# Performance work log

Measured on AMD Instinct MI355X. Metric: run time of the kernel, lower is better.

## Reference

```python
import jax, jax.numpy as jnp
import numpy as np

P_DROP = 0.2
N_NODES = 100000
N_EDGES = 1600000
IN_DIM, HID_DIM, OUT_DIM = 128, 128, 64


def sage_conv(x, src, dst, Wl, Wr, b, n_nodes):
    # PyG SAGEConv (aggr='mean', root_weight=True):
    #   out_i = W_l @ mean_{j in N(i)} x_j + W_r @ x_i + b
    msgs = jnp.take(x, src, axis=0)                                   # [E, d]
    agg = jax.ops.segment_sum(msgs, dst, num_segments=n_nodes)        # [N, d]
    cnt = jax.ops.segment_sum(jnp.ones((src.shape[0],), x.dtype), dst,
                              num_segments=n_nodes)                   # [N]
    agg = agg / jnp.maximum(cnt, 1.0)[:, None]                        # mean, 0 for isolated nodes
    return agg @ Wl + x @ Wr + b


def setup_inputs() -> dict:
    key = jax.random.key(0)
    ks = jax.random.split(key, 8)
    x = jax.random.normal(ks[0], (N_NODES, IN_DIM), dtype=jnp.float32)
    edge_index = jax.random.randint(ks[1], (2, N_EDGES), 0, N_NODES, dtype=jnp.int32)
    drop_u = jax.random.uniform(ks[2], (N_NODES, HID_DIM), dtype=jnp.float32)
    s1 = 1.0 / np.sqrt(IN_DIM)
    s2 = 1.0 / np.sqrt(HID_DIM)
    W1l = jax.random.normal(ks[3], (IN_DIM, HID_DIM), dtype=jnp.float32) * s1
    W1r = jax.random.normal(ks[4], (IN_DIM, HID_DIM), dtype=jnp.float32) * s1
    b1 = jnp.zeros((HID_DIM,), dtype=jnp.float32)
    W2l = jax.random.normal(ks[5], (HID_DIM, OUT_DIM), dtype=jnp.float32) * s2
    W2r = jax.random.normal(ks[6], (HID_DIM, OUT_DIM), dtype=jnp.float32) * s2
    b2 = jnp.zeros((OUT_DIM,), dtype=jnp.float32)
    return {"x": x, "edge_index": edge_index, "drop_u": drop_u,
            "W1l": W1l, "W1r": W1r, "b1": b1,
            "W2l": W2l, "W2r": W2r, "b2": b2}


def reference(x, edge_index, drop_u, W1l, W1r, b1, W2l, W2r, b2):
    n = x.shape[0]
    src, dst = edge_index[0], edge_index[1]
    h = jax.nn.elu(sage_conv(x, src, dst, W1l, W1r, b1, n))
    keep = (drop_u >= P_DROP).astype(h.dtype) / (1.0 - P_DROP)  # inverted dropout, p=0.2
    h = h * keep
    h = jax.nn.elu(sage_conv(h, src, dst, W2l, W2r, b2, n))
    return h
```

## Files before the change

kernel.cpp:

```cpp
#include <hip/hip_runtime.h>
#include <cstdint>
#include <cstddef>

#define TPB 256
#define BCAP 2560
#define NBKMAX 800
#define EPB 8192

typedef short bf16x8 __attribute__((ext_vector_type(8)));
typedef float f32x4 __attribute__((ext_vector_type(4)));

__device__ __forceinline__ unsigned short f2bf(float f) {
  unsigned int u = __float_as_uint(f);
  unsigned int r = (u + 0x7fffu + ((u >> 16) & 1u)) >> 16;
  return (unsigned short)r;
}
__device__ __forceinline__ float bf2f(unsigned short h) {
  return __uint_as_float(((unsigned int)h) << 16);
}

__device__ __forceinline__ float elu_neg(float v) { return __expf(v) - 1.0f; }

__device__ __forceinline__ void gload16(const void* g, void* l) {
  __builtin_amdgcn_global_load_lds(
      (const __attribute__((address_space(1))) unsigned int*)g,
      (__attribute__((address_space(3))) unsigned int*)l, 16, 0, 0);
}

template <int N>
__device__ __forceinline__ void waitvm() {
  asm volatile("s_waitcnt vmcnt(%0)" ::"n"(N) : "memory");
}


__global__ __launch_bounds__(256) void multisplit_scatter(
    const int* __restrict__ src, const int* __restrict__ dst,
    unsigned int* __restrict__ be, int* __restrict__ bcnt, int e, int nbk) {
  __shared__ int hist[NBKMAX];
  __shared__ int curs[NBKMAX];
  int tx = threadIdx.x;
  int e0 = blockIdx.x * EPB;
  int e1 = min(e, e0 + EPB);

  for (int b = tx; b < nbk; b += TPB) hist[b] = 0;
  __syncthreads();
  for (int i = e0 + tx; i < e1; i += TPB) atomicAdd(&hist[dst[i] >> 7], 1);
  __syncthreads();
  int rot = (blockIdx.x * 131) % nbk;
  for (int s = tx; s < nbk; s += TPB) {
    int b = s + rot;
    if (b >= nbk) b -= nbk;
    int h = hist[b];
    curs[b] = (h > 0) ? atomicAdd(&bcnt[b], h) : 0;
  }
  __syncthreads();
  for (int i = e0 + tx; i < e1; i += TPB) {
    int d = dst[i];
    int b = d >> 7;
    int p = atomicAdd(&curs[b], 1);
    if (p < BCAP)
      be[(size_t)b * BCAP + p] = ((unsigned int)(d & 127) << 17) | (unsigned int)src[i];
  }
}

__global__ __launch_bounds__(256) void per_bucket_build(
    const unsigned int* __restrict__ be, const int* __restrict__ bcnt,
    int* __restrict__ gcur, int* __restrict__ off, int* __restrict__ offend,
    int* __restrict__ col, int n) {
  int b = blockIdx.x, tx = threadIdx.x;
  int cnt = bcnt[b];
  if (cnt > BCAP) cnt = BCAP;
  int node0 = b << 7;
  __shared__ unsigned int stage[BCAP];
  __shared__ int ssrc[BCAP];
  __shared__ int scnt[128];
  __shared__ int sscan[128];
  __shared__ int sbase;
  if (tx < 128) scnt[tx] = 0;
  __syncthreads();
  const unsigned int* eb = be + (size_t)b * BCAP;
  for (int i = tx; i < cnt; i += 256) stage[i] = eb[i];
  __syncthreads();
  for (int i = tx; i < cnt; i += 256) atomicAdd(&scnt[stage[i] >> 17], 1);
  __syncthreads();
  if (tx < 128) sscan[tx] = scnt[tx];
  __syncthreads();
  for (int d = 1; d < 128; d <<= 1) {
    int t = 0;
    if (tx < 128 && tx >= d) t = sscan[tx - d];
    __syncthreads();
    if (tx < 128) sscan[tx] += t;
    __syncthreads();
  }
  if (tx == 0) sbase = atomicAdd(gcur, cnt);
  __syncthreads();
  int base = sbase;
  if (tx < 128) {
    int excl = sscan[tx] - scnt[tx];
    if (node0 + tx < n) {
      off[node0 + tx] = base + excl;
      offend[node0 + tx] = base + sscan[tx];
    }
    scnt[tx] = excl;
  }
  __syncthreads();
  for (int i = tx; i < cnt; i += 256) {
    unsigned int u = stage[i];
    int p = atomicAdd(&scnt[u >> 17], 1);
    ssrc[p] = (int)(u & 0x1ffff);
  }
  __syncthreads();
  for (int i = tx; i < cnt; i += 256) col[base + i] = ssrc[i];
}


__global__ void prep_all(const float* __restrict__ x, const float* __restrict__ W1l,
                         const float* __restrict__ W1r, const float* __restrict__ W2l,
                         const float* __restrict__ W2r, unsigned short* __restrict__ xb,
                         unsigned short* __restrict__ Wt1, unsigned short* __restrict__ Wt2,
                         int n4) {
  int idx = blockIdx.x * TPB + threadIdx.x;
  if (idx < n4) {
    float4 v = ((const float4*)x)[idx];
    ushort4 o;
    o.x = f2bf(v.x); o.y = f2bf(v.y); o.z = f2bf(v.z); o.w = f2bf(v.w);
    ((ushort4*)xb)[idx] = o;
    return;
  }
  int r = idx - n4;
  if (r < 128 * 256) {
    int nn = r >> 8;
    int k = r & 255;
    float v = (k < 128) ? W1l[k * 128 + nn] : W1r[(k - 128) * 128 + nn];
    Wt1[r] = f2bf(v);
    return;
  }
  r -= 128 * 256;
  if (r < 128 * 128) {
    int nn = r >> 7;
    int k = r & 127;
    float v = (nn < 64) ? W2l[k * 64 + nn] : W2r[k * 64 + (nn - 64)];
    Wt2[r] = f2bf(v);
  }
}


__global__ void aggregate_bf(const unsigned short* __restrict__ X,
                             const int* __restrict__ off, const int* __restrict__ offend,
                             const int* __restrict__ col,
                             unsigned short* __restrict__ out, int n) {
  int wv = (blockIdx.x * TPB + threadIdx.x) >> 6;
  int lane = threadIdx.x & 63;
  int li = lane & 15;
  int node = wv * 4 + (lane >> 4);
  if (node >= n) return;
  int s0 = off[node], s1 = offend[node];
  int cnt = s1 - s0;

  float a0 = 0.f, a1 = 0.f, a2 = 0.f, a3 = 0.f,
        a4 = 0.f, a5 = 0.f, a6 = 0.f, a7 = 0.f;

  for (int base = 0; base < cnt; base += 16) {
    int idx = s0 + base + li;
    int ci = col[min(idx, s1 - 1)];
    int lim = cnt - base;
#pragma unroll
    for (int j = 0; j < 16; ++j) {
      int c = __shfl(ci, j, 16);
      const uint4* p = (const uint4*)(X + (size_t)c * 128 + li * 8);
      uint4 v = *p;
      float s = (j < lim) ? 1.f : 0.f;
      a0 = fmaf(s, __uint_as_float(v.x << 16), a0);
      a1 = fmaf(s, __uint_as_float(v.x & 0xffff0000u), a1);
      a2 = fmaf(s, __uint_as_float(v.y << 16), a2);
      a3 = fmaf(s, __uint_as_float(v.y & 0xffff0000u), a3);
      a4 = fmaf(s, __uint_as_float(v.z << 16), a4);
      a5 = fmaf(s, __uint_as_float(v.z & 0xffff0000u), a5);
      a6 = fmaf(s, __uint_as_float(v.w << 16), a6);
      a7 = fmaf(s, __uint_as_float(v.w & 0xffff0000u), a7);
    }
  }

  float inv = (cnt > 0) ? 1.0f / (float)cnt : 0.f;
  uint4 o;
  o.x = ((unsigned int)f2bf(a1 * inv) << 16) | f2bf(a0 * inv);
  o.y = ((unsigned int)f2bf(a3 * inv) << 16) | f2bf(a2 * inv);
  o.z = ((unsigned int)f2bf(a5 * inv) << 16) | f2bf(a4 * inv);
  o.w = ((unsigned int)f2bf(a7 * inv) << 16) | f2bf(a6 * inv);
  *(uint4*)(out + (size_t)node * 128 + li * 8) = o;
}


__global__ void aggregate_add(const unsigned short* __restrict__ P,
                              const int* __restrict__ off, const int* __restrict__ offend,
                              const int* __restrict__ col,
                              const float* __restrict__ Q, float* __restrict__ out, int n) {
  int wv = (blockIdx.x * TPB + threadIdx.x) >> 6;
  int lane = threadIdx.x & 63;
  int li = lane & 7;
  int node = wv * 8 + (lane >> 3);
  bool alive = node < n;
  int s0 = 0, s1 = 0;
  if (alive) { s0 = off[node]; s1 = offend[node]; }
  int cnt = s1 - s0;

  float a0 = 0.f, a1 = 0.f, a2 = 0.f, a3 = 0.f,
        a4 = 0.f, a5 = 0.f, a6 = 0.f, a7 = 0.f;

  for (int base = 0; base < cnt; base += 8) {
    int ci = col[max(0, min(s0 + base + li, s1 - 1))];
    int lim = cnt - base;
#pragma unroll
    for (int j = 0; j < 8; ++j) {
      int c = __shfl(ci, j, 8);
      uint4 v = *(const uint4*)(P + (size_t)c * 64 + li * 8);
      float s = (j < lim) ? 1.f : 0.f;
      a0 = fmaf(s, __uint_as_float(v.x << 16), a0);
      a1 = fmaf(s, __uint_as_float(v.x & 0xffff0000u), a1);
      a2 = fmaf(s, __uint_as_float(v.y << 16), a2);
      a3 = fmaf(s, __uint_as_float(v.y & 0xffff0000u), a3);
      a4 = fmaf(s, __uint_as_float(v.z << 16), a4);
      a5 = fmaf(s, __uint_as_float(v.z & 0xffff0000u), a5);
      a6 = fmaf(s, __uint_as_float(v.w << 16), a6);
      a7 = fmaf(s, __uint_as_float(v.w & 0xffff0000u), a7);
    }
  }

  if (alive) {
    float inv = (cnt > 0) ? 1.0f / (float)cnt : 0.f;
    const float4* qp = (const float4*)(Q + (size_t)node * 64 + li * 8);
    float4 q0 = qp[0], q1 = qp[1];
    float4 o0, o1;
    o0.x = a0 * inv + q0.x; o0.y = a1 * inv + q0.y;
    o0.z = a2 * inv + q0.z; o0.w = a3 * inv + q0.w;
    o1.x = a4 * inv + q1.x; o1.y = a5 * inv + q1.y;
    o1.z = a6 * inv + q1.z; o1.w = a7 * inv + q1.w;
    o0.x = (o0.x > 0.f) ? o0.x : elu_neg(o0.x);
    o0.y = (o0.y > 0.f) ? o0.y : elu_neg(o0.y);
    o0.z = (o0.z > 0.f) ? o0.z : elu_neg(o0.z);
    o0.w = (o0.w > 0.f) ? o0.w : elu_neg(o0.w);
    o1.x = (o1.x > 0.f) ? o1.x : elu_neg(o1.x);
    o1.y = (o1.y > 0.f) ? o1.y : elu_neg(o1.y);
    o1.z = (o1.z > 0.f) ? o1.z : elu_neg(o1.z);
    o1.w = (o1.w > 0.f) ? o1.w : elu_neg(o1.w);
    float4* op = (float4*)(out + (size_t)node * 64 + li * 8);
    op[0] = o0; op[1] = o1;
  }
}


template <int NCH, int MODE>
__global__ __launch_bounds__(256) void gemm_mfma(
    const unsigned short* __restrict__ A1, const unsigned short* __restrict__ A2,
    const unsigned short* __restrict__ Wt, const float* __restrict__ bias,
    const float* __restrict__ drp, unsigned short* __restrict__ outb,
    float* __restrict__ outf, int n) {
  constexpr int IPC = 4;
  constexpr int KTOT = NCH * 64;
  __shared__ __align__(16) unsigned short sA[2][64 * 64];
  __shared__ __align__(16) unsigned short sB[2][64 * 64];

  int g = blockIdx.x;
  int p = (g >> 4) * 8 + (g & 7);
  int yy = (g >> 3) & 1;
  int nrb = (n + 63) >> 6;
  if (p >= nrb) return;

  int tid = threadIdx.x;
  int row0 = p * 64;
  int ncol0 = yy * 64;
  int lane = tid & 63;
  int wid = tid >> 6;
  int wm = wid >> 1, wn = wid & 1;
  int lq = lane & 15, q = lane >> 4;

  int sr = tid >> 3, sc8 = tid & 7;
  int cg = sc8 ^ (sr & 7);

  int arow[2];
#pragma unroll
  for (int t = 0; t < 2; ++t) arow[t] = min(row0 + sr + t * 32, n - 1);

  f32x4 acc[2][2];
#pragma unroll
  for (int i = 0; i < 2; ++i)
#pragma unroll
    for (int j = 0; j < 2; ++j) acc[i][j] = (f32x4)(0.f);

  auto issue = [&](int c, int b) {
    const unsigned short* Asrc = (MODE == 0 && c >= NCH / 2) ? A2 : A1;
    int koff = (MODE == 0 ? (c & (NCH / 2 - 1)) : c) * 64;
#pragma unroll
    for (int t = 0; t < 2; ++t) {
      gload16(Asrc + (size_t)arow[t] * 128 + koff + cg * 8,
              (char*)sA[b] + t * 4096 + wid * 1024);
    }
#pragma unroll
    for (int t = 0; t < 2; ++t) {
      gload16(Wt + (size_t)(ncol0 + sr + t * 32) * KTOT + c * 64 + cg * 8,
              (char*)sB[b] + t * 4096 + wid * 1024);
    }
  };

  issue(0, 0);
  issue(1, 1);

#pragma unroll
  for (int c = 0; c < NCH; ++c) {
    if (c < NCH - 1) waitvm<IPC>(); else waitvm<0>();
    __builtin_amdgcn_s_barrier();
    __builtin_amdgcn_sched_barrier(0);

    const int buf = c & 1;
#pragma unroll
    for (int ks = 0; ks < 2; ++ks) {
      bf16x8 a[2], b[2];
#pragma unroll
      for (int i = 0; i < 2; ++i) {
        int rr = wm * 32 + i * 16 + lq;
        a[i] = *(const bf16x8*)(&sA[buf][rr * 64 + (((ks * 4 + q) ^ (rr & 7)) * 8)]);
      }
#pragma unroll
      for (int j = 0; j < 2; ++j) {
        int rb = wn * 32 + j * 16 + lq;
        b[j] = *(const bf16x8*)(&sB[buf][rb * 64 + (((ks * 4 + q) ^ (rb & 7)) * 8)]);
      }
#pragma unroll
      for (int i = 0; i < 2; ++i)
#pragma unroll
        for (int j = 0; j < 2; ++j)
          acc[i][j] = __builtin_amdgcn_mfma_f32_16x16x32_bf16(a[i], b[j], acc[i][j], 0, 0, 0);
    }

    if (c < NCH - 2) {
      asm volatile("s_waitcnt lgkmcnt(0)" ::: "memory");
      __builtin_amdgcn_sched_barrier(0);
      __builtin_amdgcn_s_barrier();
      issue(c + 2, buf);
    }
  }

#pragma unroll
  for (int j = 0; j < 2; ++j) {
    int gcol = ncol0 + wn * 32 + j * 16 + lq;
    float bv;
    if (MODE == 0) bv = bias[gcol];
    else bv = (gcol >= 64) ? bias[gcol - 64] : 0.f;
#pragma unroll
    for (int i = 0; i < 2; ++i) {
      int rbase = row0 + wm * 32 + i * 16 + q * 4;
#pragma unroll
      for (int r = 0; r < 4; ++r) {
        int row = rbase + r;
        if (row >= n) continue;
        float v = acc[i][j][r] + bv;
        if (MODE == 0) {
          v = (v > 0.f) ? v : elu_neg(v);
          float u = drp[(size_t)row * 128 + gcol];
          v = (u >= 0.2f) ? v * 1.25f : 0.f;
          outb[(size_t)row * 128 + gcol] = f2bf(v);
        } else {
          if (gcol < 64) outb[(size_t)row * 64 + gcol] = f2bf(v);
          else outf[(size_t)row * 64 + (gcol - 64)] = v;
        }
      }
    }
  }
}


extern "C" void kernel_launch(void* const* d_in, const int* in_sizes, int n_in,
                              void* d_out, int out_size, void* d_ws, size_t ws_size,
                              hipStream_t stream) {
  const float* x = (const float*)d_in[0];
  const int* ei = (const int*)d_in[1];
  const float* dropu = (const float*)d_in[2];
  const float* W1l = (const float*)d_in[3];
  const float* W1r = (const float*)d_in[4];
  const float* b1 = (const float*)d_in[5];
  const float* W2l = (const float*)d_in[6];
  const float* W2r = (const float*)d_in[7];
  const float* b2 = (const float*)d_in[8];

  int n = in_sizes[0] / 128;
  int e = in_sizes[1] / 2;
  const int* src = ei;
  const int* dst = ei + e;
  float* out = (float*)d_out;

  char* w = (char*)d_ws;
  auto alloc = [&](size_t bytes) -> char* {
    char* p = w;
    w += (bytes + 255) & ~(size_t)255;
    return p;
  };
  int nbk = (n + 127) / 128;
  int* off = (int*)alloc((size_t)n * sizeof(int));
  int* offend = (int*)alloc((size_t)n * sizeof(int));
  int* col = (int*)alloc((size_t)e * sizeof(int));
  int* bcnt = (int*)alloc((size_t)(nbk + 1) * sizeof(int));
  int* gcur = bcnt + nbk;
  unsigned short* xb = (unsigned short*)alloc((size_t)n * 128 * 2);
  unsigned short* hb = (unsigned short*)alloc((size_t)n * 128 * 2);
  unsigned short* aggb = (unsigned short*)alloc((size_t)n * 128 * 2);
  unsigned short* Wt1 = (unsigned short*)alloc(128 * 256 * 2);
  unsigned short* Wt2 = (unsigned short*)alloc(128 * 128 * 2);
  unsigned int* be = (unsigned int*)aggb;
  unsigned short* pb = xb;
  float* qf = (float*)aggb;

  hipMemsetAsync(bcnt, 0, (size_t)(nbk + 1) * sizeof(int), stream);

  int gMS = (e + EPB - 1) / EPB;
  multisplit_scatter<<<gMS, TPB, 0, stream>>>(src, dst, be, bcnt, e, nbk);
  per_bucket_build<<<nbk, TPB, 0, stream>>>(be, bcnt, gcur, off, offend, col, n);

  int n4 = n * 128 / 4;
  int prepTot = n4 + 128 * 256 + 128 * 128;
  prep_all<<<(prepTot + TPB - 1) / TPB, TPB, 0, stream>>>(x, W1l, W1r, W2l, W2r,
                                                          xb, Wt1, Wt2, n4);

  int gAgg1 = ((n + 3) / 4 * 64 + TPB - 1) / TPB;
  int gAgg2 = (n + 31) / 32;
  int gR = (n + 63) / 64;
  int gG = ((gR + 7) / 8) * 16;

  aggregate_bf<<<gAgg1, TPB, 0, stream>>>(xb, off, offend, col, aggb, n);
  gemm_mfma<4, 0><<<gG, TPB, 0, stream>>>(aggb, xb, Wt1, b1, dropu, hb, nullptr, n);

  gemm_mfma<2, 1><<<gG, TPB, 0, stream>>>(hb, nullptr, Wt2, b2, nullptr, pb, qf, n);
  aggregate_add<<<gAgg2, TPB, 0, stream>>>(pb, off, offend, col, qf, out, n);
}
```

Measured before the change: 371.6 us.

## Fuse layer-1 neighbor aggregation into the MFMA GEMM via shared memory

Layer-1 mean aggregation now runs inside the GEMM kernel. Each 64-row block gathers neighbor features, writes the bf16 means straight into the swizzled LDS A-tile, and then runs MFMA over all 128 output columns. Weight tiles are prefetched while the gather runs. This removes the aggb round trip through global memory and one kernel launch. The cost is fewer blocks (one per 64 rows instead of two column halves), more LDS per block, and gather latency that may be harder to hide at lower occupancy.

```diff
diff --git a/kernel.cpp b/kernel.cpp
--- a/kernel.cpp
+++ b/kernel.cpp
@@ -145,49 +145,155 @@
 }
 
 
-__global__ void aggregate_bf(const unsigned short* __restrict__ X,
-                             const int* __restrict__ off, const int* __restrict__ offend,
-                             const int* __restrict__ col,
-                             unsigned short* __restrict__ out, int n) {
-  int wv = (blockIdx.x * TPB + threadIdx.x) >> 6;
-  int lane = threadIdx.x & 63;
+__global__ __launch_bounds__(256) void fused_l1(
+    const unsigned short* __restrict__ X,
+    const int* __restrict__ off, const int* __restrict__ offend,
+    const int* __restrict__ col,
+    const unsigned short* __restrict__ Wt,
+    const float* __restrict__ bias, const float* __restrict__ drp,
+    unsigned short* __restrict__ outb, int n) {
+  __shared__ __align__(16) unsigned short sA[2][64 * 64];
+  __shared__ __align__(16) unsigned short sB[2][128 * 64];
+
+  int tid = threadIdx.x;
+  int row0 = blockIdx.x * 64;
+  int lane = tid & 63;
+  int wid = tid >> 6;
+  int wm = wid >> 1, wn = wid & 1;
+  int lq = lane & 15, q = lane >> 4;
+
+  int sr = tid >> 3, sc8 = tid & 7;
+  int cg = sc8 ^ (sr & 7);
+
+  auto issueB = [&](int c, int b) {
+#pragma unroll
+    for (int t = 0; t < 4; ++t)
+      gload16(Wt + (size_t)(sr + t * 32) * 256 + c * 64 + cg * 8,
+              (char*)sB[b] + t * 4096 + wid * 1024);
+  };
+  auto issueA = [&](int c, int b) {
+    int koff = (c & 1) * 64;
+#pragma unroll
+    for (int t = 0; t < 2; ++t) {
+      int row = min(row0 + sr + t * 32, n - 1);
+      gload16(X + (size_t)row * 128 + koff + cg * 8,
+              (char*)sA[b] + t * 4096 + wid * 1024);
+    }
+  };
+
+  issueB(0, 0);
+  issueB(1, 1);
+
   int li = lane & 15;
-  int node = wv * 4 + (lane >> 4);
-  if (node >= n) return;
-  int s0 = off[node], s1 = offend[node];
-  int cnt = s1 - s0;
-
-  float a0 = 0.f, a1 = 0.f, a2 = 0.f, a3 = 0.f,
-        a4 = 0.f, a5 = 0.f, a6 = 0.f, a7 = 0.f;
-
-  for (int base = 0; base < cnt; base += 16) {
-    int idx = s0 + base + li;
-    int ci = col[min(idx, s1 - 1)];
-    int lim = cnt - base;
-#pragma unroll
-    for (int j = 0; j < 16; ++j) {
-      int c = __shfl(ci, j, 16);
-      const uint4* p = (const uint4*)(X + (size_t)c * 128 + li * 8);
-      uint4 v = *p;
-      float s = (j < lim) ? 1.f : 0.f;
-      a0 = fmaf(s, __uint_as_float(v.x << 16), a0);
-      a1 = fmaf(s, __uint_as_float(v.x & 0xffff0000u), a1);
-      a2 = fmaf(s, __uint_as_float(v.y << 16), a2);
-      a3 = fmaf(s, __uint_as_float(v.y & 0xffff0000u), a3);
-      a4 = fmaf(s, __uint_as_float(v.z << 16), a4);
-      a5 = fmaf(s, __uint_as_float(v.z & 0xffff0000u), a5);
-      a6 = fmaf(s, __uint_as_float(v.w << 16), a6);
-      a7 = fmaf(s, __uint_as_float(v.w & 0xffff0000u), a7);
-    }
-  }
-
-  float inv = (cnt > 0) ? 1.0f / (float)cnt : 0.f;
-  uint4 o;
-  o.x = ((unsigned int)f2bf(a1 * inv) << 16) | f2bf(a0 * inv);
-  o.y = ((unsigned int)f2bf(a3 * inv) << 16) | f2bf(a2 * inv);
-  o.z = ((unsigned int)f2bf(a5 * inv) << 16) | f2bf(a4 * inv);
-  o.w = ((unsigned int)f2bf(a7 * inv) << 16) | f2bf(a6 * inv);
-  *(uint4*)(out + (size_t)node * 128 + li * 8) = o;
+  for (int pp = 0; pp < 4; ++pp) {
+    int r = pp * 16 + wid * 4 + (lane >> 4);
+    int node = row0 + r;
+    int s0 = 0, s1 = 0;
+    if (node < n) { s0 = off[node]; s1 = offend[node]; }
+    int cnt = s1 - s0;
+
+    float a0 = 0.f, a1 = 0.f, a2 = 0.f, a3 = 0.f,
+          a4 = 0.f, a5 = 0.f, a6 = 0.f, a7 = 0.f;
+    for (int base = 0; base < cnt; base += 16) {
+      int ci = col[min(s0 + base + li, s1 - 1)];
+      int lim = cnt - base;
+#pragma unroll
+      for (int j = 0; j < 16; ++j) {
+        int c = __shfl(ci, j, 16);
+        uint4 v = *(const uint4*)(X + (size_t)c * 128 + li * 8);
+        float s = (j < lim) ? 1.f : 0.f;
+        a0 = fmaf(s, __uint_as_float(v.x << 16), a0);
+        a1 = fmaf(s, __uint_as_float(v.x & 0xffff0000u), a1);
+        a2 = fmaf(s, __uint_as_float(v.y << 16), a2);
+        a3 = fmaf(s, __uint_as_float(v.y & 0xffff0000u), a3);
+        a4 = fmaf(s, __uint_as_float(v.z << 16), a4);
+        a5 = fmaf(s, __uint_as_float(v.z & 0xffff0000u), a5);
+        a6 = fmaf(s, __uint_as_float(v.w << 16), a6);
+        a7 = fmaf(s, __uint_as_float(v.w & 0xffff0000u), a7);
+      }
+    }
+    float inv = (cnt > 0) ? 1.0f / (float)cnt : 0.f;
+    uint4 pk;
+    pk.x = ((unsigned int)f2bf(a1 * inv) << 16) | f2bf(a0 * inv);
+    pk.y = ((unsigned int)f2bf(a3 * inv) << 16) | f2bf(a2 * inv);
+    pk.z = ((unsigned int)f2bf(a5 * inv) << 16) | f2bf(a4 * inv);
+    pk.w = ((unsigned int)f2bf(a7 * inv) << 16) | f2bf(a6 * inv);
+    int c01 = li >> 3, gg = li & 7;
+    *(uint4*)(&sA[c01][r * 64 + ((gg ^ (r & 7)) * 8)]) = pk;
+  }
+
+  asm volatile("s_waitcnt lgkmcnt(0)" ::: "memory");
+  __builtin_amdgcn_sched_barrier(0);
+  waitvm<0>();
+  __builtin_amdgcn_s_barrier();
+  __builtin_amdgcn_sched_barrier(0);
+
+  f32x4 acc[2][4];
+#pragma unroll
+  for (int i = 0; i < 2; ++i)
+#pragma unroll
+    for (int j = 0; j < 4; ++j) acc[i][j] = (f32x4)(0.f);
+
+#pragma unroll
+  for (int c = 0; c < 4; ++c) {
+    if (c == 2) {
+      waitvm<6>();
+      __builtin_amdgcn_s_barrier();
+      __builtin_amdgcn_sched_barrier(0);
+    }
+    if (c == 3) {
+      waitvm<0>();
+      __builtin_amdgcn_s_barrier();
+      __builtin_amdgcn_sched_barrier(0);
+    }
+    const int buf = c & 1;
+#pragma unroll
+    for (int ks = 0; ks < 2; ++ks) {
+      bf16x8 a[2], b[4];
+#pragma unroll
+      for (int i = 0; i < 2; ++i) {
+        int rr = wm * 32 + i * 16 + lq;
+        a[i] = *(const bf16x8*)(&sA[buf][rr * 64 + (((ks * 4 + q) ^ (rr & 7)) * 8)]);
+      }
+#pragma unroll
+      for (int j = 0; j < 4; ++j) {
+        int rb = wn * 64 + j * 16 + lq;
+        b[j] = *(const bf16x8*)(&sB[buf][rb * 64 + (((ks * 4 + q) ^ (rb & 7)) * 8)]);
+      }
+#pragma unroll
+      for (int i = 0; i < 2; ++i)
+#pragma unroll
+        for (int j = 0; j < 4; ++j)
+          acc[i][j] = __builtin_amdgcn_mfma_f32_16x16x32_bf16(a[i], b[j], acc[i][j], 0, 0, 0);
+    }
+    if (c < 2) {
+      asm volatile("s_waitcnt lgkmcnt(0)" ::: "memory");
+      __builtin_amdgcn_sched_barrier(0);
+      __builtin_amdgcn_s_barrier();
+      issueA(c + 2, buf);
+      issueB(c + 2, buf);
+    }
+  }
+
+#pragma unroll
+  for (int j = 0; j < 4; ++j) {
+    int gcol = wn * 64 + j * 16 + lq;
+    float bv = bias[gcol];
+#pragma unroll
+    for (int i = 0; i < 2; ++i) {
+      int rbase = row0 + wm * 32 + i * 16 + q * 4;
+#pragma unroll
+      for (int r = 0; r < 4; ++r) {
+        int row = rbase + r;
+        if (row >= n) continue;
+        float v = acc[i][j][r] + bv;
+        v = (v > 0.f) ? v : elu_neg(v);
+        float u = drp[(size_t)row * 128 + gcol];
+        v = (u >= 0.2f) ? v * 1.25f : 0.f;
+        outb[(size_t)row * 128 + gcol] = f2bf(v);
+      }
+    }
+  }
 }
 
 
@@ -249,11 +355,10 @@
 }
 
 
-template <int NCH, int MODE>
-__global__ __launch_bounds__(256) void gemm_mfma(
-    const unsigned short* __restrict__ A1, const unsigned short* __restrict__ A2,
-    const unsigned short* __restrict__ Wt, const float* __restrict__ bias,
-    const float* __restrict__ drp, unsigned short* __restrict__ outb,
+template <int NCH>
+__global__ __launch_bounds__(256) void gemm_l2(
+    const unsigned short* __restrict__ A1, const unsigned short* __restrict__ Wt,
+    const float* __restrict__ bias, unsigned short* __restrict__ outb,
     float* __restrict__ outf, int n) {
   constexpr int IPC = 4;
   constexpr int KTOT = NCH * 64;
@@ -288,11 +393,10 @@
     for (int j = 0; j < 2; ++j) acc[i][j] = (f32x4)(0.f);
 
   auto issue = [&](int c, int b) {
-    const unsigned short* Asrc = (MODE == 0 && c >= NCH / 2) ? A2 : A1;
-    int koff = (MODE == 0 ? (c & (NCH / 2 - 1)) : c) * 64;
+    int koff = c * 64;
 #pragma unroll
     for (int t = 0; t < 2; ++t) {
-      gload16(Asrc + (size_t)arow[t] * 128 + koff + cg * 8,
+      gload16(A1 + (size_t)arow[t] * 128 + koff + cg * 8,
               (char*)sA[b] + t * 4096 + wid * 1024);
     }
 #pragma unroll
@@ -343,9 +447,7 @@
 #pragma unroll
   for (int j = 0; j < 2; ++j) {
     int gcol = ncol0 + wn * 32 + j * 16 + lq;
-    float bv;
-    if (MODE == 0) bv = bias[gcol];
-    else bv = (gcol >= 64) ? bias[gcol - 64] : 0.f;
+    float bv = (gcol >= 64) ? bias[gcol - 64] : 0.f;
 #pragma unroll
     for (int i = 0; i < 2; ++i) {
       int rbase = row0 + wm * 32 + i * 16 + q * 4;
@@ -354,15 +456,8 @@
         int row = rbase + r;
         if (row >= n) continue;
         float v = acc[i][j][r] + bv;
-        if (MODE == 0) {
-          v = (v > 0.f) ? v : elu_neg(v);
-          float u = drp[(size_t)row * 128 + gcol];
-          v = (u >= 0.2f) ? v * 1.25f : 0.f;
-          outb[(size_t)row * 128 + gcol] = f2bf(v);
-        } else {
-          if (gcol < 64) outb[(size_t)row * 64 + gcol] = f2bf(v);
-          else outf[(size_t)row * 64 + (gcol - 64)] = v;
-        }
+        if (gcol < 64) outb[(size_t)row * 64 + gcol] = f2bf(v);
+        else outf[(size_t)row * 64 + (gcol - 64)] = v;
       }
     }
   }
@@ -420,14 +515,12 @@
   prep_all<<<(prepTot + TPB - 1) / TPB, TPB, 0, stream>>>(x, W1l, W1r, W2l, W2r,
                                                           xb, Wt1, Wt2, n4);
 
-  int gAgg1 = ((n + 3) / 4 * 64 + TPB - 1) / TPB;
   int gAgg2 = (n + 31) / 32;
-  int gR = (n + 63) / 64;
-  int gG = ((gR + 7) / 8) * 16;
-
-  aggregate_bf<<<gAgg1, TPB, 0, stream>>>(xb, off, offend, col, aggb, n);
-  gemm_mfma<4, 0><<<gG, TPB, 0, stream>>>(aggb, xb, Wt1, b1, dropu, hb, nullptr, n);
-
-  gemm_mfma<2, 1><<<gG, TPB, 0, stream>>>(hb, nullptr, Wt2, b2, nullptr, pb, qf, n);
+  int gR64 = (n + 63) / 64;
+  int gG = ((gR64 + 7) / 8) * 16;
+
+  fused_l1<<<gR64, TPB, 0, stream>>>(xb, off, offend, col, Wt1, b1, dropu, hb, n);
+
+  gemm_l2<2><<<gG, TPB, 0, stream>>>(hb, Wt2, b2, pb, qf, n);
   aggregate_add<<<gAgg2, TPB, 0, stream>>>(pb, off, offend, col, qf, out, n);
 }
```

After: 413.4 us. 11.3% more time.
